# Performance work log

Hardware: AMD Instinct MI355X
Metric: run time of the kernel (lower is better)

The kernel has to match this reference:

```python
import jax, jax.numpy as jnp
import numpy as np

EPS = 1e-12  # numerical floor inside sqrt for grad stability


def _mean_p2cp(u, v):
    """Mean point-to-closest-point distance.
    u: [..., n, 2] predicted curve points, v: [..., m, 2] target curve points.
    Returns [...] symmetric mean-of-min distances, matching
    MeanP2CPDistance: (min over v per u-point).mean + (min over u per v-point).mean, halved.
    Uses the gram-matrix form of cdist to avoid a [..., n, m, 2] diff tensor.
    """
    u2 = jnp.sum(u * u, axis=-1)                      # [..., n]
    v2 = jnp.sum(v * v, axis=-1)                      # [..., m]
    gram = jnp.einsum('...ik,...jk->...ij', u, v)     # [..., n, m]
    d2 = jnp.maximum(u2[..., :, None] + v2[..., None, :] - 2.0 * gram, 0.0)
    d = jnp.sqrt(d2 + EPS)                            # [..., n, m] pairwise euclidean
    u2v = jnp.min(d, axis=-1).mean(axis=-1)           # for each u point, closest v point
    v2u = jnp.min(d, axis=-2).mean(axis=-1)           # for each v point, closest u point
    return 0.5 * (u2v + v2u)


def setup_inputs() -> dict:
    key = jax.random.key(0)
    k1, k2, k3, k4 = jax.random.split(key, 4)
    bs, seq_len, n_components, n_samples = 8, 512, 12, 128
    outputs = jax.random.normal(k1, (bs, seq_len, n_components), dtype=jnp.float32)
    targets = jax.random.normal(k2, (bs, seq_len, 1, 2, n_samples), dtype=jnp.float32)
    W_dec = jax.random.normal(k3, (n_components, 2 * n_samples), dtype=jnp.float32) * 0.1
    b_dec = jax.random.normal(k4, (2 * n_samples,), dtype=jnp.float32) * 0.01
    return {"outputs": outputs, "targets": targets, "W_dec": W_dec, "b_dec": b_dec}


def reference(outputs, targets, W_dec, b_dec):
    bs, seq_len, n_art, _, n_samples = targets.shape
    # Decode: linear PCA-style decoder n_components -> 2*n_samples
    shapes = outputs @ W_dec + b_dec                       # [bs, seq, 2*n_samples]
    u = shapes.reshape(bs, seq_len, 1, 2, n_samples)       # unsqueeze(2) equivalent
    u = jnp.swapaxes(u, -1, -2)                            # permute(0,1,2,4,3) -> [bs,seq,1,n,2]
    v = jnp.swapaxes(targets, -1, -2)                      # [bs,seq,n_art,n,2]
    p2cp = _mean_p2cp(u, v)                                # [bs,seq,n_art]
    return jnp.mean(p2cp)                                  # reduction='mean'
```

## Files before the change

kernel.cpp:

```cpp
#include <hip/hip_runtime.h>
#include <math.h>
#include <float.h>

#define NCOMP 12
#define NS 128
#define NBS 4096
#define WPB 4

typedef float f32x2 __attribute__((ext_vector_type(2)));
typedef float f32x4 __attribute__((ext_vector_type(4)));

__device__ __forceinline__ f32x4 shfl_xor4(f32x4 v, int mask) {
    f32x4 r;
    r.x = __shfl_xor(v.x, mask);
    r.y = __shfl_xor(v.y, mask);
    r.z = __shfl_xor(v.z, mask);
    r.w = __shfl_xor(v.w, mask);
    return r;
}

__global__ __launch_bounds__(256)
void p2cp_wave_kernel(const float* __restrict__ outputs,
                      const float* __restrict__ targets,
                      const float* __restrict__ W_dec,
                      const float* __restrict__ b_dec,
                      float* __restrict__ partial) {
    const int wav  = threadIdx.x >> 6;
    const int lane = threadIdx.x & 63;
    const int bsq  = blockIdx.x * WPB + wav;

    __shared__ __align__(16) f32x4 c4s[WPB][2][NS / 2];
    __shared__ __align__(16) float zzs[WPB][2][NS];
    f32x4 (*c4)[NS / 2] = c4s[wav];
    float (*zw)[NS]     = zzs[wav];

    const int half = lane >> 5;
    const int m    = lane & 31;

    const float* ob = outputs + (size_t)bsq * NCOMP;
    const f32x4 o0 = *reinterpret_cast<const f32x4*>(ob);
    const f32x4 o1 = *reinterpret_cast<const f32x4*>(ob + 4);
    const f32x4 o2 = *reinterpret_cast<const f32x4*>(ob + 8);

    f32x4 du = *reinterpret_cast<const f32x4*>(b_dec + 4 * lane);
    const float* wb = W_dec + 4 * lane;
    #pragma unroll
    for (int k = 0; k < 4; ++k)
        du += o0[k] * *reinterpret_cast<const f32x4*>(wb + (k    ) * 256);
    #pragma unroll
    for (int k = 0; k < 4; ++k)
        du += o1[k] * *reinterpret_cast<const f32x4*>(wb + (k + 4) * 256);
    #pragma unroll
    for (int k = 0; k < 4; ++k)
        du += o2[k] * *reinterpret_cast<const f32x4*>(wb + (k + 8) * 256);

    const float* tb = targets + (size_t)bsq * (2 * NS);
    const f32x4 dv = *reinterpret_cast<const f32x4*>(tb + 4 * lane);

    const f32x4 pu = shfl_xor4(du, 32);
    const f32x4 pv = shfl_xor4(dv, 32);
    const f32x4 ox = half ? pv : du;
    const f32x4 oy = half ? dv : pu;
    f32x4 zz4;
    #pragma unroll
    for (int c = 0; c < 4; ++c) zz4[c] = fmaf(ox[c], ox[c], oy[c] * oy[c]);

    {
        float* u0 = reinterpret_cast<float*>(&c4[0][2 * m])     + 2 * half;
        float* u1 = reinterpret_cast<float*>(&c4[0][2 * m + 1]) + 2 * half;
        float* v0 = reinterpret_cast<float*>(&c4[1][2 * m])     + 2 * half;
        float* v1 = reinterpret_cast<float*>(&c4[1][2 * m + 1]) + 2 * half;
        *reinterpret_cast<f32x2*>(u0) = f32x2{du.x, du.y};
        *reinterpret_cast<f32x2*>(u1) = f32x2{du.z, du.w};
        *reinterpret_cast<f32x2*>(v0) = f32x2{dv.x, dv.y};
        *reinterpret_cast<f32x2*>(v1) = f32x2{dv.z, dv.w};
        *reinterpret_cast<f32x4*>(&zw[half][4 * m]) = zz4;
    }
    asm volatile("s_waitcnt lgkmcnt(0)" ::: "memory");
    __builtin_amdgcn_sched_barrier(0);

    const f32x4* cp = c4[1 - half];
    const float* zp = zw[1 - half];

    f32x2 ab[4];
    float mn[4];
    #pragma unroll
    for (int k = 0; k < 4; ++k) {
        ab[k] = f32x2{-2.0f * ox[k], -2.0f * oy[k]};
        mn[k] = FLT_MAX;
    }

    #pragma unroll 8
    for (int i = 0; i < NS / 2; ++i) {
        const f32x4 q  = cp[i];
        const f32x2 z2 = *reinterpret_cast<const f32x2*>(zp + 2 * i);
        f32x2 xx; xx.x = q.x; xx.y = q.y;
        f32x2 yy; yy.x = q.z; yy.y = q.w;
        #pragma unroll
        for (int k = 0; k < 4; ++k) {
            f32x2 t1, dd;
            asm("v_pk_fma_f32 %0, %1, %2, %3 op_sel:[1,0,0] op_sel_hi:[1,1,1]"
                : "=v"(t1) : "v"(ab[k]), "v"(yy), "v"(z2));
            asm("v_pk_fma_f32 %0, %1, %2, %3 op_sel:[0,0,0] op_sel_hi:[0,1,1]"
                : "=v"(dd) : "v"(ab[k]), "v"(xx), "v"(t1));
            asm("v_min3_f32 %0, %1, %2, %3"
                : "=v"(mn[k]) : "v"(mn[k]), "v"(dd.x), "v"(dd.y));
        }
    }

    float s = 0.0f;
    #pragma unroll
    for (int k = 0; k < 4; ++k) {
        const float d2 = fmaxf(mn[k] + zz4[k], 0.0f);
        s += sqrtf(d2 + 1e-12f);
    }
    #pragma unroll
    for (int off = 32; off > 0; off >>= 1)
        s += __shfl_xor(s, off);
    if (lane == 0)
        partial[bsq] = s;
}

__global__ __launch_bounds__(256)
void final_reduce_kernel(const float* __restrict__ partial,
                         float* __restrict__ out) {
    const int t = threadIdx.x;
    float s = 0.0f;
    #pragma unroll
    for (int i = 0; i < 16; ++i) s += partial[t + 256 * i];
    #pragma unroll
    for (int off = 32; off > 0; off >>= 1)
        s += __shfl_down(s, off);
    __shared__ float red[4];
    const int lane = t & 63;
    const int wid  = t >> 6;
    if (lane == 0) red[wid] = s;
    __syncthreads();
    if (t == 0) {
        const float total = red[0] + red[1] + red[2] + red[3];
        out[0] = total * (1.0f / (256.0f * (float)NBS));
    }
}

extern "C" void kernel_launch(void* const* d_in, const int* in_sizes, int n_in,
                              void* d_out, int out_size, void* d_ws, size_t ws_size,
                              hipStream_t stream) {
    const float* outputs = (const float*)d_in[0];
    const float* targets = (const float*)d_in[1];
    const float* W_dec   = (const float*)d_in[2];
    const float* b_dec   = (const float*)d_in[3];
    float* out = (float*)d_out;
    float* ws  = (float*)d_ws;

    p2cp_wave_kernel<<<NBS / WPB, 256, 0, stream>>>(outputs, targets, W_dec, b_dec, ws);
    final_reduce_kernel<<<1, 256, 0, stream>>>(ws, out);
}
```

Before: 17.39 us.

## Split candidate scan across wave halves with 8 owned points per lane

Each lane now owns 8 points instead of 4 and scans only half of the opposite curve's points, 32 iterations instead of 64. The two halves' partial minima are merged with one cross-half shuffle. The squared norms are computed in registers instead of being stored to and read back from LDS, which removes the zz shared array and the setup shuffles. The result is half as many LDS loads in the inner loop at the cost of extra packed FMAs per iteration to recompute candidate norms. Because every point is now summed twice, the final normalisation divisor is doubled to match.

```diff
diff --git a/kernel.cpp b/kernel.cpp
--- a/kernel.cpp
+++ b/kernel.cpp
@@ -10,15 +10,6 @@
 typedef float f32x2 __attribute__((ext_vector_type(2)));
 typedef float f32x4 __attribute__((ext_vector_type(4)));
 
-__device__ __forceinline__ f32x4 shfl_xor4(f32x4 v, int mask) {
-    f32x4 r;
-    r.x = __shfl_xor(v.x, mask);
-    r.y = __shfl_xor(v.y, mask);
-    r.z = __shfl_xor(v.z, mask);
-    r.w = __shfl_xor(v.w, mask);
-    return r;
-}
-
 __global__ __launch_bounds__(256)
 void p2cp_wave_kernel(const float* __restrict__ outputs,
                       const float* __restrict__ targets,
@@ -30,9 +21,7 @@
     const int bsq  = blockIdx.x * WPB + wav;
 
     __shared__ __align__(16) f32x4 c4s[WPB][2][NS / 2];
-    __shared__ __align__(16) float zzs[WPB][2][NS];
     f32x4 (*c4)[NS / 2] = c4s[wav];
-    float (*zw)[NS]     = zzs[wav];
 
     const int half = lane >> 5;
     const int m    = lane & 31;
@@ -57,14 +46,6 @@
     const float* tb = targets + (size_t)bsq * (2 * NS);
     const f32x4 dv = *reinterpret_cast<const f32x4*>(tb + 4 * lane);
 
-    const f32x4 pu = shfl_xor4(du, 32);
-    const f32x4 pv = shfl_xor4(dv, 32);
-    const f32x4 ox = half ? pv : du;
-    const f32x4 oy = half ? dv : pu;
-    f32x4 zz4;
-    #pragma unroll
-    for (int c = 0; c < 4; ++c) zz4[c] = fmaf(ox[c], ox[c], oy[c] * oy[c]);
-
     {
         float* u0 = reinterpret_cast<float*>(&c4[0][2 * m])     + 2 * half;
         float* u1 = reinterpret_cast<float*>(&c4[0][2 * m + 1]) + 2 * half;
@@ -74,30 +55,40 @@
         *reinterpret_cast<f32x2*>(u1) = f32x2{du.z, du.w};
         *reinterpret_cast<f32x2*>(v0) = f32x2{dv.x, dv.y};
         *reinterpret_cast<f32x2*>(v1) = f32x2{dv.z, dv.w};
-        *reinterpret_cast<f32x4*>(&zw[half][4 * m]) = zz4;
     }
     asm volatile("s_waitcnt lgkmcnt(0)" ::: "memory");
     __builtin_amdgcn_sched_barrier(0);
 
-    const f32x4* cp = c4[1 - half];
-    const float* zp = zw[1 - half];
+    const int g = lane & 31;
+    const int h = g & 15;
+    const int sideOwn = (g < 16) ? 0 : 1;
 
-    f32x2 ab[4];
-    float mn[4];
+    f32x2 ab[8];
+    float zown[8], mn[8];
     #pragma unroll
-    for (int k = 0; k < 4; ++k) {
-        ab[k] = f32x2{-2.0f * ox[k], -2.0f * oy[k]};
-        mn[k] = FLT_MAX;
+    for (int j = 0; j < 4; ++j) {
+        const int q = 4 * h + ((j + (h >> 1)) & 3);
+        const f32x4 P = c4[sideOwn][q];
+        ab[2 * j]     = f32x2{-2.0f * P.x, -2.0f * P.z};
+        ab[2 * j + 1] = f32x2{-2.0f * P.y, -2.0f * P.w};
+        zown[2 * j]     = fmaf(P.x, P.x, P.z * P.z);
+        zown[2 * j + 1] = fmaf(P.y, P.y, P.w * P.w);
+        mn[2 * j] = FLT_MAX; mn[2 * j + 1] = FLT_MAX;
     }
 
+    const f32x4* cp = c4[1 - sideOwn];
+    const int pbase = 32 * half;
+    const int stag  = sideOwn ? 4 : 0;
+
     #pragma unroll 8
-    for (int i = 0; i < NS / 2; ++i) {
-        const f32x4 q  = cp[i];
-        const f32x2 z2 = *reinterpret_cast<const f32x2*>(zp + 2 * i);
-        f32x2 xx; xx.x = q.x; xx.y = q.y;
-        f32x2 yy; yy.x = q.z; yy.y = q.w;
+    for (int i = 0; i < 32; ++i) {
+        const int p = ((i + stag) & 31) + pbase;
+        const f32x4 qq = cp[p];
+        f32x2 xx; xx.x = qq.x; xx.y = qq.y;
+        f32x2 yy; yy.x = qq.z; yy.y = qq.w;
+        const f32x2 z2 = xx * xx + yy * yy;
         #pragma unroll
-        for (int k = 0; k < 4; ++k) {
+        for (int k = 0; k < 8; ++k) {
             f32x2 t1, dd;
             asm("v_pk_fma_f32 %0, %1, %2, %3 op_sel:[1,0,0] op_sel_hi:[1,1,1]"
                 : "=v"(t1) : "v"(ab[k]), "v"(yy), "v"(z2));
@@ -108,10 +99,14 @@
         }
     }
 
+    #pragma unroll
+    for (int k = 0; k < 8; ++k)
+        mn[k] = fminf(mn[k], __shfl_xor(mn[k], 32));
+
     float s = 0.0f;
     #pragma unroll
-    for (int k = 0; k < 4; ++k) {
-        const float d2 = fmaxf(mn[k] + zz4[k], 0.0f);
+    for (int k = 0; k < 8; ++k) {
+        const float d2 = fmaxf(mn[k] + zown[k], 0.0f);
         s += sqrtf(d2 + 1e-12f);
     }
     #pragma unroll
@@ -138,7 +133,7 @@
     __syncthreads();
     if (t == 0) {
         const float total = red[0] + red[1] + red[2] + red[3];
-        out[0] = total * (1.0f / (256.0f * (float)NBS));
+        out[0] = total * (1.0f / (512.0f * (float)NBS));
     }
 }
 
```

Measured after the change: 19.44 us. 11.8% more time.
